# Kernel tuning notes

Hardware: AMD Instinct MI355X
Metric: run time of the kernel (lower is better)

The kernel has to match this reference:

```python
import jax, jax.numpy as jnp
import numpy as np

NU = 256      # numunits
NH = 32       # torch.split chunk size == head dim in this code
B = 128
S = 256


def _linear_tanh(x, W, b):
    # torch nn.Linear: y = x @ W.T + b, followed by tanh
    return jnp.tanh(x @ W.T + b)


def _split_heads(x):
    # torch.split(x, NH, dim=-1) then cat(dim=0): chunk c occupies rows [c*B, (c+1)*B)
    b, s, d = x.shape
    c = d // NH
    return x.reshape(b, s, c, NH).transpose(2, 0, 1, 3).reshape(c * b, s, NH)


def _merge_heads(x, b):
    # torch.split(x, batchsize, dim=0) then cat(dim=-1): inverse of _split_heads
    cb, s, hd = x.shape
    c = cb // b
    return x.reshape(c, b, s, hd).transpose(1, 2, 0, 3).reshape(b, s, c * hd)


def _attention(Q, K, V):
    d_k = jnp.asarray(K.shape[2], Q.dtype) ** 0.5
    scores = jnp.einsum('nqd,nkd->nqk', Q, K) / d_k
    # NB: original uses F.softmax(scores) with no dim on a 3D tensor ->
    # torch legacy default is dim=0. We reproduce that exactly.
    p_attn = jax.nn.softmax(scores, axis=0)
    return jnp.einsum('nqk,nkd->nqd', p_attn, V)


def setup_inputs() -> dict:
    key = jax.random.key(0)
    ks = jax.random.split(key, 24)
    def w(k):
        return jax.random.normal(k, (NU, NU), dtype=jnp.float32) * 0.02
    def bvec(k):
        return jax.random.normal(k, (NU,), dtype=jnp.float32) * 0.02
    inp = {
        'queries1': jax.random.normal(ks[0], (B, S, NU), dtype=jnp.float32),
        'queries2': jax.random.normal(ks[1], (B, S, NU), dtype=jnp.float32),
        'queries3': jax.random.normal(ks[2], (B, S, NU), dtype=jnp.float32),
        'adj': jax.random.randint(ks[3], (B,), 0, B, dtype=jnp.int64),
        'WQ': w(ks[4]),  'bQ': bvec(ks[5]),
        'WV': w(ks[6]),  'bV': bvec(ks[7]),
        'WQ3': w(ks[8]), 'bQ3': bvec(ks[9]),
        'WK3': w(ks[10]), 'bK3': bvec(ks[11]),
        'WV3': w(ks[12]), 'bV3': bvec(ks[13]),
        'WQ4': w(ks[14]), 'bQ4': bvec(ks[15]),
        'WV4': w(ks[16]), 'bV4': bvec(ks[17]),
        'W5': jax.random.normal(ks[18], (NU, 4 * NU), dtype=jnp.float32) * 0.02,
        'b5': bvec(ks[19]),
    }
    return inp


def reference(queries1, queries2, queries3, adj,
              WQ, bQ, WV, bV, WQ3, bQ3, WK3, bK3, WV3, bV3,
              WQ4, bQ4, WV4, bV4, W5, b5):
    b = queries1.shape[0]
    # per-row batch gather: queries4[i] = queries3[adj[i]]
    queries4 = queries3[adj]

    Q1 = _split_heads(_linear_tanh(queries1, WQ, bQ))
    Q2 = _split_heads(_linear_tanh(queries2, WQ, bQ))
    Q3 = _split_heads(_linear_tanh(queries3, WQ3, bQ3))
    Q4 = _split_heads(_linear_tanh(queries4, WQ4, bQ4))
    K3 = _split_heads(_linear_tanh(queries3, WK3, bK3))
    V1 = _split_heads(_linear_tanh(queries1, WV, bV))
    V2 = _split_heads(_linear_tanh(queries2, WV, bV))
    V3 = _split_heads(_linear_tanh(queries3, WV3, bV3))
    V4 = _split_heads(_linear_tanh(queries4, WV4, bV4))

    o1 = _merge_heads(_attention(Q1, K3, V1), b)
    o2 = _merge_heads(_attention(Q2, K3, V2), b)
    o3 = _merge_heads(_attention(Q3, K3, V3), b)
    o4 = _merge_heads(_attention(Q4, K3, V4), b)

    o5 = jnp.tanh(jnp.concatenate([o1, o2, o3, o4], axis=-1) @ W5.T + b5)
    return (o1, o2, o5, o3)
```

## Files before the change

### kernel.cpp

```cpp
#include <hip/hip_runtime.h>


typedef __attribute__((ext_vector_type(4))) float f32x4;
typedef __attribute__((ext_vector_type(8))) short bf16x8;

#define LOG2E 1.4426950408889634f
#define SM_SCALE (1.4426950408889634f / 5.656854249492381f)

#define CVT_PK(d, lo, hi) \
    asm("v_cvt_pk_bf16_f32 %0, %1, %2" : "=v"(d) : "v"(lo), "v"(hi))
#define SWAP32(x, y) \
    asm("v_permlane32_swap_b32 %0, %1" : "+v"(x), "+v"(y))
#define SWAP16(x, y) \
    asm("v_permlane16_swap_b32 %0, %1" : "+v"(x), "+v"(y))

__device__ __forceinline__ unsigned short f2bf(float x) {
    union { float f; unsigned u; } v; v.f = x;
    unsigned r = v.u + 0x7FFFu + ((v.u >> 16) & 1u);
    return (unsigned short)(r >> 16);
}

__device__ __forceinline__ float fast_tanh(float x) {
    float e = __builtin_amdgcn_exp2f(x * (2.0f * LOG2E));
    return 1.0f - 2.0f * __builtin_amdgcn_rcpf(e + 1.0f);
}

__device__ __forceinline__ f32x4 mfma_bf16(bf16x8 a, bf16x8 b, f32x4 c) {
    return __builtin_amdgcn_mfma_f32_16x16x32_bf16(a, b, c, 0, 0, 0);
}

__global__ __launch_bounds__(256) void k_convert_w(
    const float* w0, const float* w1, const float* w2, const float* w3,
    const float* w4, const float* w5, const float* w6, const float* w7,
    unsigned short* out)
{
    int i = blockIdx.x * 256 + threadIdx.x;
    if (i >= 720896) return;
    float v;
    if (i < 458752) {
        int r = i >> 16, j = i & 65535;
        const float* s =
            (r == 0) ? w0 : (r == 1) ? w1 : (r == 2) ? w2 :
            (r == 3) ? w3 : (r == 4) ? w4 : (r == 5) ? w5 : w6;
        v = s[j];
    } else {
        v = w7[i - 458752];
    }
    out[i] = (short)f2bf(v);
}

__global__ __launch_bounds__(256) void k_convert_x(
    const float* __restrict__ q1, const float* __restrict__ q2,
    const float* __restrict__ q3, unsigned short* __restrict__ Xb)
{
    const int gi = (blockIdx.x * 256 + threadIdx.x) * 8;
    const float* s = (gi < 8388608) ? q1 : (gi < 16777216) ? q2 : q3;
    const int off = gi & 8388607;
    float4 f0 = *(const float4*)(s + off);
    float4 f1 = *(const float4*)(s + off + 4);
    unsigned a0, a1, a2, a3;
    CVT_PK(a0, f0.x, f0.y);
    CVT_PK(a1, f0.z, f0.w);
    CVT_PK(a2, f1.x, f1.y);
    CVT_PK(a3, f1.z, f1.w);
    uint4 pk; pk.x = a0; pk.y = a1; pk.z = a2; pk.w = a3;
    *(uint4*)(Xb + gi) = pk;
}

__global__ __launch_bounds__(512, 4) void k_linear(
    const unsigned short* __restrict__ Xb, const int* __restrict__ adj,
    const unsigned short* __restrict__ wb,
    const float* __restrict__ bQ, const float* __restrict__ bV,
    const float* __restrict__ bQ3, const float* __restrict__ bK3,
    const float* __restrict__ bV3, const float* __restrict__ bQ4,
    const float* __restrict__ bV4,
    unsigned short* __restrict__ lin)
{
    __shared__ __align__(16) short lds[30720];
    const int bid0 = blockIdx.x;
    const int swz = (bid0 & 7) * 320 + (bid0 >> 3);
    const int var = swz >> 9;
    const int rem = swz & 511;
    const int m0 = (rem >> 1) * 128, n0 = (rem & 1) * 128;

    const unsigned short* X = Xb + (size_t)((var == 0) ? 0 : (var == 1) ? 1 : 2) * 8388608;
    const bool gather = (var == 4);
    const int nout = (var == 3) ? 1 : 2;

    int widx0, widx1 = 0, zidx0, zidx1 = 0;
    const float* bp0;
    const float* bp1 = bQ;
    if (var == 0)      { widx0=0; widx1=1; zidx0=0; zidx1=5; bp0=bQ;  bp1=bV;  }
    else if (var == 1) { widx0=0; widx1=1; zidx0=1; zidx1=6; bp0=bQ;  bp1=bV;  }
    else if (var == 2) { widx0=2; widx1=3; zidx0=2; zidx1=4; bp0=bQ3; bp1=bK3; }
    else if (var == 3) { widx0=4;          zidx0=7;          bp0=bV3;          }
    else               { widx0=5; widx1=6; zidx0=3; zidx1=8; bp0=bQ4; bp1=bV4; }

    const int tid = threadIdx.x;
    const int w = tid >> 6, l = tid & 63;
    const int wm = w >> 2, wn = w & 3;
    const int lr = l & 15, lk = (l >> 4) * 8, lq = (l >> 4) * 4;

    const int srow = tid >> 2, scol = (tid & 3) * 8;
    const int gm = m0 + srow;
    const int sm = gather ? (adj[gm >> 8] * 256 + (gm & 255)) : gm;
    const unsigned short* aSrc = X + (size_t)sm * 256 + scol;
    const unsigned short* b0Src = wb + (size_t)widx0 * 65536 + (size_t)(n0 + srow) * 256 + scol;
    const unsigned short* b1Src = wb + (size_t)widx1 * 65536 + (size_t)(n0 + srow) * 256 + scol;

    bf16x8 ar, b0r, b1r;
    f32x4 acc[2][4][2] = {};

    ar = *(const bf16x8*)(aSrc);
    b0r = *(const bf16x8*)(b0Src);
    if (nout == 2) b1r = *(const bf16x8*)(b1Src);
    *(bf16x8*)&lds[srow * 40 + scol] = ar;
    *(bf16x8*)&lds[5120 + srow * 40 + scol] = b0r;
    if (nout == 2) *(bf16x8*)&lds[10240 + srow * 40 + scol] = b1r;
    ar = *(const bf16x8*)(aSrc + 32);
    b0r = *(const bf16x8*)(b0Src + 32);
    if (nout == 2) b1r = *(const bf16x8*)(b1Src + 32);
    __syncthreads();

    for (int st = 0; st < 8; ++st) {
        const int p = st & 1;
        const short* base = lds + p * 15360;
        bf16x8 af[4], bf0[2], bf1[2];
        #pragma unroll
        for (int i = 0; i < 4; ++i)
            af[i] = *(const bf16x8*)&base[(wm * 64 + i * 16 + lr) * 40 + lk];
        #pragma unroll
        for (int j = 0; j < 2; ++j)
            bf0[j] = *(const bf16x8*)&base[5120 + (wn * 32 + j * 16 + lr) * 40 + lk];
        if (nout == 2)
            #pragma unroll
            for (int j = 0; j < 2; ++j)
                bf1[j] = *(const bf16x8*)&base[10240 + (wn * 32 + j * 16 + lr) * 40 + lk];
        #pragma unroll
        for (int i = 0; i < 4; ++i)
            #pragma unroll
            for (int j = 0; j < 2; ++j)
                acc[0][i][j] = mfma_bf16(af[i], bf0[j], acc[0][i][j]);
        if (nout == 2)
            #pragma unroll
            for (int i = 0; i < 4; ++i)
                #pragma unroll
                for (int j = 0; j < 2; ++j)
                    acc[1][i][j] = mfma_bf16(af[i], bf1[j], acc[1][i][j]);
        if (st < 7) {
            short* nbase = lds + (p ^ 1) * 15360;
            *(bf16x8*)&nbase[srow * 40 + scol] = ar;
            *(bf16x8*)&nbase[5120 + srow * 40 + scol] = b0r;
            if (nout == 2) *(bf16x8*)&nbase[10240 + srow * 40 + scol] = b1r;
            if (st < 6) {
                const int ko = (st + 2) * 32;
                ar = *(const bf16x8*)(aSrc + ko);
                b0r = *(const bf16x8*)(b0Src + ko);
                if (nout == 2) b1r = *(const bf16x8*)(b1Src + ko);
            }
        }
        __syncthreads();
    }

    #pragma unroll
    for (int t = 0; t < 2; ++t)
        if (t < nout) {
            const float* bp = t ? bp1 : bp0;
            float bv[2];
            #pragma unroll
            for (int j = 0; j < 2; ++j)
                bv[j] = bp[n0 + wn * 32 + j * 16 + lr];
            #pragma unroll
            for (int i = 0; i < 4; ++i)
                #pragma unroll
                for (int j = 0; j < 2; ++j)
                    #pragma unroll
                    for (int r = 0; r < 4; ++r)
                        lds[(wm * 64 + i * 16 + lq + r) * 136 + wn * 32 + j * 16 + lr] =
                            (short)f2bf(fast_tanh(acc[t][i][j][r] + bv[j]));
            __syncthreads();
            unsigned short* Y = lin + (size_t)(t ? zidx1 : zidx0) * 8388608;
            #pragma unroll
            for (int it2 = 0; it2 < 4; ++it2) {
                const int c = tid + it2 * 512;
                const int row = c >> 4, col8 = (c & 15) * 8;
                *(bf16x8*)(Y + (size_t)(m0 + row) * 256 + n0 + col8) =
                    *(const bf16x8*)&lds[row * 136 + col8];
            }
            __syncthreads();
        }
}

__global__ __launch_bounds__(256) void k_denom(
    const unsigned short* __restrict__ Qa, const unsigned short* __restrict__ Qb2,
    const unsigned short* __restrict__ Qc, const unsigned short* __restrict__ Qd,
    const unsigned short* __restrict__ Kb, float* __restrict__ partialBase)
{
    __shared__ __align__(16) short Qs[2][128 * 40];
    __shared__ __align__(16) short Ks[2][128 * 40];
    const int tid = threadIdx.x, w = tid >> 6, l = tid & 63;
    const int q0 = (blockIdx.x >> 1) * 128, k0 = (blockIdx.x & 1) * 128;
    const int g = blockIdx.y, a = blockIdx.z;
    const unsigned short* Qb = (a == 0) ? Qa : (a == 1) ? Qb2 : (a == 2) ? Qc : Qd;
    float* partial = partialBase + ((size_t)a * 32 + g) * 65536;
    const int lr = l & 15, lk = (l >> 4) * 8, lq = (l >> 4) * 4;

    f32x4 eacc[2][8] = {};
    for (int it = 0; it < 32; it += 2) {
        __syncthreads();
        #pragma unroll
        for (int u = 0; u < 2; ++u) {
            const int n = g * 32 + it + u;
            const int c = n >> 7, b = n & 127;
            const size_t base = (size_t)b * 65536 + (size_t)c * 32;
            for (int ci = tid; ci < 512; ci += 256) {
                int r = ci >> 2, ch = ci & 3;
                *(bf16x8*)&Qs[u][r * 40 + ch * 8] =
                    *(const bf16x8*)(Qb + base + (size_t)(q0 + r) * 256 + ch * 8);
                *(bf16x8*)&Ks[u][r * 40 + ch * 8] =
                    *(const bf16x8*)(Kb + base + (size_t)(k0 + r) * 256 + ch * 8);
            }
        }
        __syncthreads();
        #pragma unroll
        for (int u = 0; u < 2; ++u) {
            bf16x8 aq[2], bk[8];
            #pragma unroll
            for (int i = 0; i < 2; ++i)
                aq[i] = *(const bf16x8*)&Qs[u][(w * 32 + i * 16 + lr) * 40 + lk];
            #pragma unroll
            for (int j = 0; j < 8; ++j)
                bk[j] = *(const bf16x8*)&Ks[u][(j * 16 + lr) * 40 + lk];
            #pragma unroll
            for (int i = 0; i < 2; ++i)
                #pragma unroll
                for (int j = 0; j < 8; ++j) {
                    f32x4 s = mfma_bf16(aq[i], bk[j], (f32x4){0.f, 0.f, 0.f, 0.f});
                    #pragma unroll
                    for (int r = 0; r < 4; ++r)
                        eacc[i][j][r] += __builtin_amdgcn_exp2f(s[r] * SM_SCALE);
                }
        }
    }
    #pragma unroll
    for (int i = 0; i < 2; ++i)
        #pragma unroll
        for (int j = 0; j < 8; ++j)
            #pragma unroll
            for (int r = 0; r < 4; ++r) {
                int q = q0 + w * 32 + i * 16 + lq + r;
                int k = k0 + j * 16 + lr;
                partial[(size_t)q * 256 + k] = eacc[i][j][r];
            }
}

__global__ __launch_bounds__(256) void k_reduce(
    const float* __restrict__ partial, float* __restrict__ dinvP)
{
    int a = blockIdx.y;
    int i = blockIdx.x * 256 + threadIdx.x;
    const float* p = partial + (size_t)a * 32 * 65536 + i;
    float s = 0.f;
    #pragma unroll
    for (int g = 0; g < 32; ++g) s += p[(size_t)g * 65536];
    const int q = i >> 8, k = i & 255;
    const int w_ = q >> 6, iq = (q >> 4) & 3, q16 = q & 15;
    const int kp = k >> 5, j = (k >> 4) & 1, h = (k >> 2) & 3, r = k & 3;
    const int off = (((((((w_ * 8 + kp) * 4 + iq) * 2 + j) * 4 + h) * 16) + q16) * 4) + r;
    dinvP[((size_t)a << 16) + off] = 1.0f / s;
}

__global__ __launch_bounds__(256) void k_attn(
    const unsigned short* __restrict__ Q1, const unsigned short* __restrict__ Q2,
    const unsigned short* __restrict__ Q3, const unsigned short* __restrict__ Q4,
    const unsigned short* __restrict__ Kb,
    const unsigned short* __restrict__ V1, const unsigned short* __restrict__ V2,
    const unsigned short* __restrict__ V3, const unsigned short* __restrict__ V4,
    const float* __restrict__ dinvP,
    float* __restrict__ outBase, unsigned short* __restrict__ ob4)
{
    __shared__ __align__(16) short Vt[32 * 264];
    const int tid = threadIdx.x, w = tid >> 6, l = tid & 63;
    const int bid = blockIdx.x;
    const int swz = (bid & 7) * 512 + (bid >> 3);
    const int a = swz & 3, n = swz >> 2;
    const int c = n >> 7, b = n & 127;
    const int q16 = l & 15, h = l >> 4;
    const size_t base = (size_t)b * 65536 + (size_t)c * 32;

    const unsigned short* Qb = (a == 0) ? Q1 : (a == 1) ? Q2 : (a == 2) ? Q3 : Q4;
    const unsigned short* Vb = (a == 0) ? V1 : (a == 1) ? V2 : (a == 2) ? V3 : V4;
    const f32x4* dpa = (const f32x4*)(dinvP + ((size_t)a << 16)) + l;
    float* outp = outBase + (size_t)((a == 2) ? 3 : a) * 8388608;

    {
        const unsigned short* vp = Vb + base + (size_t)tid * 256;
        bf16x8 v0 = *(const bf16x8*)(vp);
        bf16x8 v1 = *(const bf16x8*)(vp + 8);
        bf16x8 v2 = *(const bf16x8*)(vp + 16);
        bf16x8 v3 = *(const bf16x8*)(vp + 24);
        #pragma unroll
        for (int e = 0; e < 8; ++e) {
            Vt[(0  + e) * 264 + tid] = v0[e];
            Vt[(8  + e) * 264 + tid] = v1[e];
            Vt[(16 + e) * 264 + tid] = v2[e];
            Vt[(24 + e) * 264 + tid] = v3[e];
        }
    }
    __syncthreads();

    const int q0 = w * 64;
    bf16x8 bq[4];
    #pragma unroll
    for (int i = 0; i < 4; ++i)
        bq[i] = *(const bf16x8*)(Qb + base + (size_t)(q0 + i * 16 + q16) * 256 + h * 8);

    const unsigned short* kSrc = Kb + base + (size_t)q16 * 256 + h * 8;
    bf16x8 akA = *(const bf16x8*)(kSrc);
    bf16x8 akB = *(const bf16x8*)(kSrc + 16 * 256);

    f32x4 oacc[4][2] = {};
    for (int kp = 0; kp < 8; ++kp) {
        const int kk0 = kp * 32;
        bf16x8 nA = akA, nB = akB;
        if (kp < 7) {
            nA = *(const bf16x8*)(kSrc + (size_t)(kk0 + 32) * 256);
            nB = *(const bf16x8*)(kSrc + (size_t)(kk0 + 48) * 256);
        }
        bf16x8 vb0 = *(const bf16x8*)&Vt[(0  + q16) * 264 + kk0 + h * 8];
        bf16x8 vb1 = *(const bf16x8*)&Vt[(16 + q16) * 264 + kk0 + h * 8];
        #pragma unroll
        for (int i = 0; i < 4; ++i) {
            f32x4 s0 = mfma_bf16(akA, bq[i], (f32x4){0.f, 0.f, 0.f, 0.f});
            f32x4 s1 = mfma_bf16(akB, bq[i], (f32x4){0.f, 0.f, 0.f, 0.f});
            const int X = ((w * 8 + kp) * 4 + i) * 2;
            f32x4 d0 = dpa[(size_t)X * 64];
            f32x4 d1 = dpa[(size_t)(X + 1) * 64];
            float p0 = __builtin_amdgcn_exp2f(s0[0] * SM_SCALE) * d0[0];
            float p1 = __builtin_amdgcn_exp2f(s0[1] * SM_SCALE) * d0[1];
            float p2 = __builtin_amdgcn_exp2f(s0[2] * SM_SCALE) * d0[2];
            float p3 = __builtin_amdgcn_exp2f(s0[3] * SM_SCALE) * d0[3];
            float p4 = __builtin_amdgcn_exp2f(s1[0] * SM_SCALE) * d1[0];
            float p5 = __builtin_amdgcn_exp2f(s1[1] * SM_SCALE) * d1[1];
            float p6 = __builtin_amdgcn_exp2f(s1[2] * SM_SCALE) * d1[2];
            float p7 = __builtin_amdgcn_exp2f(s1[3] * SM_SCALE) * d1[3];
            unsigned r0, r1, r2, r3;
            CVT_PK(r0, p0, p1);
            CVT_PK(r1, p2, p3);
            CVT_PK(r2, p4, p5);
            CVT_PK(r3, p6, p7);
            SWAP32(r0, r2); SWAP16(r0, r2);
            SWAP32(r1, r3); SWAP16(r1, r3);
            union { unsigned u[4]; bf16x8 v; } F;
            F.u[0] = r0; F.u[1] = r1; F.u[2] = r2; F.u[3] = r3;
            oacc[i][0] = mfma_bf16(F.v, vb0, oacc[i][0]);
            oacc[i][1] = mfma_bf16(F.v, vb1, oacc[i][1]);
        }
        akA = nA; akB = nB;
    }
    if (a == 3) {
        #pragma unroll
        for (int i = 0; i < 4; ++i)
            #pragma unroll
            for (int d = 0; d < 2; ++d)
                #pragma unroll
                for (int r = 0; r < 4; ++r) {
                    int q = q0 + i * 16 + h * 4 + r;
                    int dc = d * 16 + q16;
                    ob4[(size_t)b * 65536 + (size_t)q * 256 + c * 32 + dc] =
                        f2bf(oacc[i][d][r]);
                }
    } else {
        #pragma unroll
        for (int i = 0; i < 4; ++i)
            #pragma unroll
            for (int d = 0; d < 2; ++d)
                #pragma unroll
                for (int r = 0; r < 4; ++r) {
                    int q = q0 + i * 16 + h * 4 + r;
                    int dc = d * 16 + q16;
                    outp[(size_t)b * 65536 + (size_t)q * 256 + c * 32 + dc] =
                        oacc[i][d][r];
                }
    }
}

__global__ __launch_bounds__(256) void k_final(
    const float* __restrict__ p0, const float* __restrict__ p1,
    const float* __restrict__ p2, const unsigned short* __restrict__ p3,
    const unsigned short* __restrict__ W5b, const float* __restrict__ b5,
    float* __restrict__ out)
{
    __shared__ __align__(16) short As[128 * 72];
    __shared__ __align__(16) short Bs[128 * 72];
    const int tid = threadIdx.x, w = tid >> 6, l = tid & 63;
    const int n0 = blockIdx.x * 128, m0 = blockIdx.y * 128;
    const int lr = l & 15, lk = (l >> 4) * 8, lq = (l >> 4) * 4;
    const int wr = (w >> 1) * 64, wc = (w & 1) * 64;
    f32x4 acc[4][4] = {};
    for (int step = 0; step < 16; ++step) {
        const int k0 = step * 64;
        const int kc = k0 & 255;
        __syncthreads();
        if (step < 12) {
            const float* P = (step < 4) ? p0 : (step < 8) ? p1 : p2;
            for (int ci = tid; ci < 1024; ci += 256) {
                int r = ci >> 3, ch = ci & 7;
                const float* src = P + (size_t)(m0 + r) * 256 + kc + ch * 8;
                float4 f0 = *(const float4*)src;
                float4 f1 = *(const float4*)(src + 4);
                unsigned a0, a1, a2, a3;
                CVT_PK(a0, f0.x, f0.y);
                CVT_PK(a1, f0.z, f0.w);
                CVT_PK(a2, f1.x, f1.y);
                CVT_PK(a3, f1.z, f1.w);
                uint4 pk; pk.x = a0; pk.y = a1; pk.z = a2; pk.w = a3;
                *(uint4*)&As[r * 72 + ch * 8] = pk;
                *(bf16x8*)&Bs[r * 72 + ch * 8] =
                    *(const bf16x8*)(W5b + (size_t)(n0 + r) * 1024 + k0 + ch * 8);
            }
        } else {
            for (int ci = tid; ci < 1024; ci += 256) {
                int r = ci >> 3, ch = ci & 7;
                *(bf16x8*)&As[r * 72 + ch * 8] =
                    *(const bf16x8*)(p3 + (size_t)(m0 + r) * 256 + kc + ch * 8);
                *(bf16x8*)&Bs[r * 72 + ch * 8] =
                    *(const bf16x8*)(W5b + (size_t)(n0 + r) * 1024 + k0 + ch * 8);
            }
        }
        __syncthreads();
        #pragma unroll
        for (int kk = 0; kk < 2; ++kk) {
            bf16x8 af[4], bfr[4];
            #pragma unroll
            for (int i = 0; i < 4; ++i)
                af[i] = *(const bf16x8*)&As[(wr + i * 16 + lr) * 72 + kk * 32 + lk];
            #pragma unroll
            for (int j = 0; j < 4; ++j)
                bfr[j] = *(const bf16x8*)&Bs[(wc + j * 16 + lr) * 72 + kk * 32 + lk];
            #pragma unroll
            for (int i = 0; i < 4; ++i)
                #pragma unroll
                for (int j = 0; j < 4; ++j)
                    acc[i][j] = mfma_bf16(af[i], bfr[j], acc[i][j]);
        }
    }
    #pragma unroll
    for (int j = 0; j < 4; ++j) {
        int col = n0 + wc + j * 16 + lr;
        float bv = b5[col];
        #pragma unroll
        for (int i = 0; i < 4; ++i) {
            int rowb = m0 + wr + i * 16 + lq;
            #pragma unroll
            for (int r = 0; r < 4; ++r)
                out[(size_t)(rowb + r) * 256 + col] =
                    fast_tanh(acc[i][j][r] + bv);
        }
    }
}

extern "C" void kernel_launch(void* const* d_in, const int* in_sizes, int n_in,
                              void* d_out, int out_size, void* d_ws, size_t ws_size,
                              hipStream_t stream)
{
    const float* q1  = (const float*)d_in[0];
    const float* q2  = (const float*)d_in[1];
    const float* q3  = (const float*)d_in[2];
    const int*   adj = (const int*)d_in[3];
    const float* WQ  = (const float*)d_in[4];  const float* bQ  = (const float*)d_in[5];
    const float* WV  = (const float*)d_in[6];  const float* bV  = (const float*)d_in[7];
    const float* WQ3 = (const float*)d_in[8];  const float* bQ3 = (const float*)d_in[9];
    const float* WK3 = (const float*)d_in[10]; const float* bK3 = (const float*)d_in[11];
    const float* WV3 = (const float*)d_in[12]; const float* bV3 = (const float*)d_in[13];
    const float* WQ4 = (const float*)d_in[14]; const float* bQ4 = (const float*)d_in[15];
    const float* WV4 = (const float*)d_in[16]; const float* bV4 = (const float*)d_in[17];
    const float* W5  = (const float*)d_in[18]; const float* b5  = (const float*)d_in[19];

    char* ws = (char*)d_ws;
    unsigned short* wb  = (unsigned short*)ws;
    unsigned short* W5b = wb + 458752;
    unsigned short* lin = (unsigned short*)(ws + 1441792);
    unsigned short* Q1 = lin + 0ull * 8388608;
    unsigned short* Q2 = lin + 1ull * 8388608;
    unsigned short* Q3 = lin + 2ull * 8388608;
    unsigned short* Q4 = lin + 3ull * 8388608;
    unsigned short* K3 = lin + 4ull * 8388608;
    unsigned short* V1 = lin + 5ull * 8388608;
    unsigned short* V2 = lin + 6ull * 8388608;
    unsigned short* V3 = lin + 7ull * 8388608;
    unsigned short* V4 = lin + 8ull * 8388608;
    float* partial = (float*)(ws + 152436736);
    float* dinvP   = (float*)(ws + 185991168);
    unsigned short* ob4 = (unsigned short*)(ws + 152436736);

    float* outf = (float*)d_out;
    float* o5p = outf + 2ull * 8388608;
    unsigned short* Xb = (unsigned short*)d_out;

    dim3 blk(256);

    hipLaunchKernelGGL(k_convert_w, dim3(2816), blk, 0, stream,
                       WQ, WV, WQ3, WK3, WV3, WQ4, WV4, W5, wb);
    hipLaunchKernelGGL(k_convert_x, dim3(12288), blk, 0, stream,
                       q1, q2, q3, Xb);

    hipLaunchKernelGGL(k_linear, dim3(2560), dim3(512), 0, stream,
                       Xb, adj, wb,
                       bQ, bV, bQ3, bK3, bV3, bQ4, bV4, lin);

    hipLaunchKernelGGL(k_denom, dim3(4, 32, 4), blk, 0, stream,
                       Q1, Q2, Q3, Q4, K3, partial);
    hipLaunchKernelGGL(k_reduce, dim3(256, 4), blk, 0, stream, partial, dinvP);

    hipLaunchKernelGGL(k_attn, dim3(4096), blk, 0, stream,
                       Q1, Q2, Q3, Q4, K3, V1, V2, V3, V4, dinvP,
                       outf, ob4);

    hipLaunchKernelGGL(k_final, dim3(2, 256), blk, 0, stream,
                       outf, outf + 8388608ull, outf + 3ull * 8388608, ob4,
                       W5b, b5, o5p);
}
```

Baseline: 335.1 us.

## Share softmax denominators across two heads per block via LDS staging

New measurement: 336.7 us. Within noise of the previous version (+0.5%).

```diff
diff --git a/kernel.cpp b/kernel.cpp
--- a/kernel.cpp
+++ b/kernel.cpp
@@ -266,11 +266,11 @@
     const int q = i >> 8, k = i & 255;
     const int w_ = q >> 6, iq = (q >> 4) & 3, q16 = q & 15;
     const int kp = k >> 5, j = (k >> 4) & 1, h = (k >> 2) & 3, r = k & 3;
-    const int off = (((((((w_ * 8 + kp) * 4 + iq) * 2 + j) * 4 + h) * 16) + q16) * 4) + r;
+    const int off = kp * 8192 + w_ * 2048 + iq * 512 + j * 256 + h * 64 + q16 * 4 + r;
     dinvP[((size_t)a << 16) + off] = 1.0f / s;
 }
 
-__global__ __launch_bounds__(256) void k_attn(
+__global__ __launch_bounds__(512, 4) void k_attn(
     const unsigned short* __restrict__ Q1, const unsigned short* __restrict__ Q2,
     const unsigned short* __restrict__ Q3, const unsigned short* __restrict__ Q4,
     const unsigned short* __restrict__ Kb,
@@ -279,37 +279,42 @@
     const float* __restrict__ dinvP,
     float* __restrict__ outBase, unsigned short* __restrict__ ob4)
 {
-    __shared__ __align__(16) short Vt[32 * 264];
+    __shared__ __align__(16) short Vt[2][32 * 264];
+    __shared__ __align__(16) float Ds[8192];
     const int tid = threadIdx.x, w = tid >> 6, l = tid & 63;
     const int bid = blockIdx.x;
-    const int swz = (bid & 7) * 512 + (bid >> 3);
-    const int a = swz & 3, n = swz >> 2;
+    const int swz = (bid & 7) * 256 + (bid >> 3);
+    const int a = swz & 3, pair = swz >> 2;
+    const int hh = w >> 2, wq = w & 3;
+    const int n = pair * 2 + hh;
     const int c = n >> 7, b = n & 127;
     const int q16 = l & 15, h = l >> 4;
     const size_t base = (size_t)b * 65536 + (size_t)c * 32;
 
     const unsigned short* Qb = (a == 0) ? Q1 : (a == 1) ? Q2 : (a == 2) ? Q3 : Q4;
     const unsigned short* Vb = (a == 0) ? V1 : (a == 1) ? V2 : (a == 2) ? V3 : V4;
-    const f32x4* dpa = (const f32x4*)(dinvP + ((size_t)a << 16)) + l;
+    const float* dvg = dinvP + ((size_t)a << 16);
     float* outp = outBase + (size_t)((a == 2) ? 3 : a) * 8388608;
 
     {
-        const unsigned short* vp = Vb + base + (size_t)tid * 256;
+        const int vh = tid >> 8, kr = tid & 255;
+        const int nv = pair * 2 + vh, cv = nv >> 7, bv = nv & 127;
+        const unsigned short* vp = Vb + (size_t)bv * 65536 + (size_t)cv * 32 +
+                                   (size_t)kr * 256;
         bf16x8 v0 = *(const bf16x8*)(vp);
         bf16x8 v1 = *(const bf16x8*)(vp + 8);
         bf16x8 v2 = *(const bf16x8*)(vp + 16);
         bf16x8 v3 = *(const bf16x8*)(vp + 24);
         #pragma unroll
         for (int e = 0; e < 8; ++e) {
-            Vt[(0  + e) * 264 + tid] = v0[e];
-            Vt[(8  + e) * 264 + tid] = v1[e];
-            Vt[(16 + e) * 264 + tid] = v2[e];
-            Vt[(24 + e) * 264 + tid] = v3[e];
-        }
-    }
-    __syncthreads();
-
-    const int q0 = w * 64;
+            Vt[vh][(0  + e) * 264 + kr] = v0[e];
+            Vt[vh][(8  + e) * 264 + kr] = v1[e];
+            Vt[vh][(16 + e) * 264 + kr] = v2[e];
+            Vt[vh][(24 + e) * 264 + kr] = v3[e];
+        }
+    }
+
+    const int q0 = wq * 64;
     bf16x8 bq[4];
     #pragma unroll
     for (int i = 0; i < 4; ++i)
@@ -319,23 +324,38 @@
     bf16x8 akA = *(const bf16x8*)(kSrc);
     bf16x8 akB = *(const bf16x8*)(kSrc + 16 * 256);
 
+    f32x4 dsr[4];
+    #pragma unroll
+    for (int it = 0; it < 4; ++it)
+        dsr[it] = *(const f32x4*)(dvg + (size_t)(tid + it * 512) * 4);
+
     f32x4 oacc[4][2] = {};
     for (int kp = 0; kp < 8; ++kp) {
+        __syncthreads();
+        #pragma unroll
+        for (int it = 0; it < 4; ++it)
+            *(f32x4*)&Ds[(tid + it * 512) * 4] = dsr[it];
+        if (kp < 7)
+            #pragma unroll
+            for (int it = 0; it < 4; ++it)
+                dsr[it] = *(const f32x4*)(dvg + (size_t)(kp + 1) * 8192 +
+                                          (size_t)(tid + it * 512) * 4);
+        __syncthreads();
+
         const int kk0 = kp * 32;
         bf16x8 nA = akA, nB = akB;
         if (kp < 7) {
             nA = *(const bf16x8*)(kSrc + (size_t)(kk0 + 32) * 256);
             nB = *(const bf16x8*)(kSrc + (size_t)(kk0 + 48) * 256);
         }
-        bf16x8 vb0 = *(const bf16x8*)&Vt[(0  + q16) * 264 + kk0 + h * 8];
-        bf16x8 vb1 = *(const bf16x8*)&Vt[(16 + q16) * 264 + kk0 + h * 8];
+        bf16x8 vb0 = *(const bf16x8*)&Vt[hh][(0  + q16) * 264 + kk0 + h * 8];
+        bf16x8 vb1 = *(const bf16x8*)&Vt[hh][(16 + q16) * 264 + kk0 + h * 8];
         #pragma unroll
         for (int i = 0; i < 4; ++i) {
             f32x4 s0 = mfma_bf16(akA, bq[i], (f32x4){0.f, 0.f, 0.f, 0.f});
             f32x4 s1 = mfma_bf16(akB, bq[i], (f32x4){0.f, 0.f, 0.f, 0.f});
-            const int X = ((w * 8 + kp) * 4 + i) * 2;
-            f32x4 d0 = dpa[(size_t)X * 64];
-            f32x4 d1 = dpa[(size_t)(X + 1) * 64];
+            f32x4 d0 = *(const f32x4*)&Ds[wq * 2048 + i * 512 + l * 4];
+            f32x4 d1 = *(const f32x4*)&Ds[wq * 2048 + i * 512 + 256 + l * 4];
             float p0 = __builtin_amdgcn_exp2f(s0[0] * SM_SCALE) * d0[0];
             float p1 = __builtin_amdgcn_exp2f(s0[1] * SM_SCALE) * d0[1];
             float p2 = __builtin_amdgcn_exp2f(s0[2] * SM_SCALE) * d0[2];
@@ -513,7 +533,7 @@
                        Q1, Q2, Q3, Q4, K3, partial);
     hipLaunchKernelGGL(k_reduce, dim3(256, 4), blk, 0, stream, partial, dinvP);
 
-    hipLaunchKernelGGL(k_attn, dim3(4096), blk, 0, stream,
+    hipLaunchKernelGGL(k_attn, dim3(2048), dim3(512), 0, stream,
                        Q1, Q2, Q3, Q4, K3, V1, V2, V3, V4, dinvP,
                        outf, ob4);
 
```
